# Optimization experiments

Hardware: AMD Instinct MI355X
Metric: run time of the kernel (lower is better)

## Reference

```python
import jax, jax.numpy as jnp
import numpy as np

STEP_SIZE = 0.1
FLOW_STRENGTH = 5.0
MAX_STEPS = 16  # points in [0,1)^2 -> max dist sqrt(2) -> at most floor(14.14)+1 = 15 steps
NNODES = 1024


def setup_inputs() -> dict:
    key = jax.random.key(0)
    ks = jax.random.split(key, 7)
    def lin(k, fan_in, shape):
        bound = 1.0 / np.sqrt(fan_in)
        return jax.random.uniform(k, shape, jnp.float32, -bound, bound)
    return {
        "embedded_points": jax.random.uniform(ks[0], (NNODES, 2), jnp.float32),
        "W1": lin(ks[1], 2, (2, 10)),  "b1": lin(ks[2], 2, (10,)),
        "W2": lin(ks[3], 10, (10, 10)), "b2": lin(ks[4], 10, (10,)),
        "W3": lin(ks[5], 10, (10, 2)),  "b3": lin(ks[6], 10, (2,)),
    }


def _flowfield(x, W1, b1, W2, b2, W3, b3):
    h = jnp.tanh(x @ W1 + b1)
    h = jnp.tanh(h @ W2 + b2)
    return h @ W3 + b3


def reference(embedded_points, W1, b1, W2, b2, W3, b3):
    # Pairwise path-integral cost matrix embedding_D[i, j] = cost(x_i, x_j)
    x1 = embedded_points[:, None, :]            # [n,1,2]
    x2 = embedded_points[None, :, :]            # [1,n,2]
    delta = x2 - x1                              # [n,n,2]
    euc = jnp.linalg.norm(delta, axis=-1)        # [n,n]
    safe_euc = jnp.where(euc > 0, euc, 1.0)
    unit = delta / safe_euc[..., None]           # [n,n,2]

    t = jnp.arange(MAX_STEPS, dtype=embedded_points.dtype)   # [S]
    # steps_to_x2: x1 + t * step_size * (x2-x1)/||x2-x1||   -> [n,n,S,2]
    steps = x1[:, :, None, :] + (t[:, None] * STEP_SIZE) * unit[:, :, None, :]

    flow = _flowfield(steps, W1, b1, W2, b2, W3, b3)          # [n,n,S,2]
    dot = jnp.einsum("ijsd,ijd->ijs", flow, delta)            # [n,n,S]
    e = jnp.exp(dot)
    cost_normalizer = FLOW_STRENGTH * e / (FLOW_STRENGTH - 1.0 + e)
    per_step = STEP_SIZE / cost_normalizer                    # [n,n,S]

    # original loops t in range(int(euc/step_size)+1): valid iff t <= floor(euc/step_size)
    n_valid = jnp.floor(euc / STEP_SIZE)                      # [n,n]
    valid = t[None, None, :] <= n_valid[..., None]            # [n,n,S]
    cost = jnp.sum(jnp.where(valid, per_step, 0.0), axis=-1)  # [n,n]
    # torch.allclose(x1, x2) -> cost 0 (identical points)
    return jnp.where(euc > 0, cost, 0.0)
```

## Files before the change

### kernel.cpp

```cpp
#include <hip/hip_runtime.h>

typedef float v2 __attribute__((ext_vector_type(2)));

constexpr int NN = 1024;
constexpr int GC = 64;
constexpr float GS = 64.0f;
constexpr int NC = GC * GC;

__device__ __forceinline__ v2 splat2(float a) { v2 r; r.x = a; r.y = a; return r; }

__device__ __forceinline__ float fast_tanh(float x) {
    float e = exp2f(x * 2.88539008177792681472f);
    return 1.0f - 2.0f * __builtin_amdgcn_rcpf(1.0f + e);
}

__device__ __forceinline__ v2 mlp_eval(float x, float y,
    const float* __restrict__ W1, const float* __restrict__ b1,
    const float* __restrict__ W2, const float* __restrict__ b2,
    const float* __restrict__ W3, const float* __restrict__ b3)
{
    float h1[10], h2[10];
#pragma unroll
    for (int k = 0; k < 10; ++k)
        h1[k] = fast_tanh(fmaf(x, W1[k], fmaf(y, W1[10 + k], b1[k])));
#pragma unroll
    for (int k = 0; k < 10; ++k) {
        float acc = b2[k];
#pragma unroll
        for (int l = 0; l < 10; ++l) acc = fmaf(h1[l], W2[10 * l + k], acc);
        h2[k] = fast_tanh(acc);
    }
    float f0 = b3[0], f1 = b3[1];
#pragma unroll
    for (int k = 0; k < 10; ++k) {
        f0 = fmaf(h2[k], W3[2 * k], f0);
        f1 = fmaf(h2[k], W3[2 * k + 1], f1);
    }
    v2 r; r.x = f0; r.y = f1;
    return r;
}

__global__ __launch_bounds__(256) void cells_kernel(
    const float* __restrict__ W1, const float* __restrict__ b1,
    const float* __restrict__ W2, const float* __restrict__ b2,
    const float* __restrict__ W3, const float* __restrict__ b3,
    v2* __restrict__ g)
{
    const int c = blockIdx.x * 256 + threadIdx.x;
    if (c >= NC) return;
    const int ix = c & (GC - 1), iy = c >> 6;
    const float x0 = (float)ix * (1.0f / GS), x1 = (float)(ix + 1) * (1.0f / GS);
    const float y0 = (float)iy * (1.0f / GS), y1 = (float)(iy + 1) * (1.0f / GS);

    const v2 f00 = mlp_eval(x0, y0, W1, b1, W2, b2, W3, b3);
    const v2 f10 = mlp_eval(x1, y0, W1, b1, W2, b2, W3, b3);
    const v2 f01 = mlp_eval(x0, y1, W1, b1, W2, b2, W3, b3);

    g[c]          = f00;
    g[NC + c]     = f10 - f00;
    g[2 * NC + c] = f01 - f00;
}

__global__ __launch_bounds__(1024) void flow_kernel(
    const float* __restrict__ pts,
    const v2* __restrict__ g,
    float* __restrict__ out)
{
    __shared__ v2 tab[3 * NC];

    const int t = threadIdx.x;
    {
        const float4* gs = (const float4*)g;
        float4* ls = (float4*)tab;
#pragma unroll
        for (int k = 0; k < 6; ++k)
            ls[t + 1024 * k] = gs[t + 1024 * k];
    }
    __syncthreads();

    const float x2x = pts[2 * t], x2y = pts[2 * t + 1];

#pragma unroll 1
    for (int q = 0; q < 4; ++q) {
        const int i = (blockIdx.x << 2) + q;
        const float x1x = pts[2 * i], x1y = pts[2 * i + 1];
        const float dx = x2x - x1x, dy = x2y - x1y;

        const float nrm2 = __fadd_rn(__fmul_rn(dx, dx), __fmul_rn(dy, dy));
        const float euc  = __fsqrt_rn(nrm2);
        const float se   = (euc > 0.0f) ? euc : 1.0f;
        const float ux   = __fdiv_rn(dx, se), uy = __fdiv_rn(dy, se);
        const int   nvi  = (int)floorf(__fdiv_rn(euc, 0.1f));
        const int   smax = (nvi < 15) ? nvi : 15;

        float pu = x1x * GS, pv = x1y * GS;
        const float du = 6.4f * ux, dv = 6.4f * uy;
        const float dxe = -1.44269504088896340736f * dx;
        const float dye = -1.44269504088896340736f * dy;

        float cost = 0.0f;
#pragma unroll 1
        for (int s = 0; s <= smax; ++s) {
            int ix = (int)pu; ix = (ix < GC - 1) ? ix : (GC - 1);
            int iy = (int)pv; iy = (iy < GC - 1) ? iy : (GC - 1);
            const float tx = pu - (float)ix;
            const float ty = pv - (float)iy;

            const int c = (iy << 6) + ix;
            const v2 a   = tab[c];
            const v2 gdx = tab[NC + c];
            const v2 gdy = tab[2 * NC + c];
            const v2 f = a + splat2(tx) * gdx + splat2(ty) * gdy;

            const float de = fmaf(f.x, dxe, f.y * dye);
            cost += fmaf(0.08f, exp2f(de), 0.02f);

            pu += du; pv += dv;
        }

        out[(i << 10) | t] = (euc > 0.0f) ? cost : 0.0f;
    }
}

extern "C" void kernel_launch(void* const* d_in, const int* in_sizes, int n_in,
                              void* d_out, int out_size, void* d_ws, size_t ws_size,
                              hipStream_t stream) {
    const float* pts = (const float*)d_in[0];
    const float* W1  = (const float*)d_in[1];
    const float* b1  = (const float*)d_in[2];
    const float* W2  = (const float*)d_in[3];
    const float* b2  = (const float*)d_in[4];
    const float* W3  = (const float*)d_in[5];
    const float* b3  = (const float*)d_in[6];
    float* out = (float*)d_out;

    v2* g = (v2*)d_ws;

    cells_kernel<<<NC / 256, 256, 0, stream>>>(W1, b1, W2, b2, W3, b3, g);
    flow_kernel<<<NN / 4, 1024, 0, stream>>>(pts, g, out);
}
```

Baseline: 23.47 us.

## Sort per-block pairs by step count to reduce warp divergence

```diff
diff --git a/kernel.cpp b/kernel.cpp
--- a/kernel.cpp
+++ b/kernel.cpp
@@ -67,23 +67,58 @@
     float* __restrict__ out)
 {
     __shared__ v2 tab[3 * NC];
+    __shared__ v2 ptsL[NN];
+    __shared__ unsigned short ordQ[4 * NN];
+    __shared__ int hist[16];
+    __shared__ int base[16];
 
     const int t = threadIdx.x;
+
     {
         const float4* gs = (const float4*)g;
         float4* ls = (float4*)tab;
 #pragma unroll
         for (int k = 0; k < 6; ++k)
             ls[t + 1024 * k] = gs[t + 1024 * k];
+        ptsL[t] = ((const v2*)pts)[t];
+    }
+    if (t < 16) hist[t] = 0;
+    __syncthreads();
+
+    int myKey[4];
+#pragma unroll
+    for (int q = 0; q < 4; ++q) {
+        const int i = (blockIdx.x << 2) + q;
+        const float ddx = ptsL[t].x - ptsL[i].x;
+        const float ddy = ptsL[t].y - ptsL[i].y;
+        const float n2 = __fadd_rn(__fmul_rn(ddx, ddx), __fmul_rn(ddy, ddy));
+        const float e  = __fsqrt_rn(n2);
+        const int  nv  = (int)floorf(__fdiv_rn(e, 0.1f));
+        myKey[q] = (nv < 15) ? nv : 15;
+        atomicAdd(&hist[myKey[q]], 1);
+    }
+    __syncthreads();
+    if (t == 0) {
+        int acc = 0;
+#pragma unroll
+        for (int k = 0; k < 16; ++k) { base[k] = acc; acc += hist[k]; }
+    }
+    __syncthreads();
+#pragma unroll
+    for (int q = 0; q < 4; ++q) {
+        const int rank = atomicAdd(&base[myKey[q]], 1);
+        ordQ[rank] = (unsigned short)((q << 10) | t);
     }
     __syncthreads();
 
-    const float x2x = pts[2 * t], x2y = pts[2 * t + 1];
+#pragma unroll 1
+    for (int r = 0; r < 4; ++r) {
+        const int item = ordQ[(r << 10) + t];
+        const int q = item >> 10, jj = item & (NN - 1);
+        const int i = (blockIdx.x << 2) + q;
 
-#pragma unroll 1
-    for (int q = 0; q < 4; ++q) {
-        const int i = (blockIdx.x << 2) + q;
-        const float x1x = pts[2 * i], x1y = pts[2 * i + 1];
+        const float x1x = ptsL[i].x,  x1y = ptsL[i].y;
+        const float x2x = ptsL[jj].x, x2y = ptsL[jj].y;
         const float dx = x2x - x1x, dy = x2y - x1y;
 
         const float nrm2 = __fadd_rn(__fmul_rn(dx, dx), __fmul_rn(dy, dy));
@@ -118,7 +153,7 @@
             pu += du; pv += dv;
         }
 
-        out[(i << 10) | t] = (euc > 0.0f) ? cost : 0.0f;
+        out[(i << 10) | jj] = (euc > 0.0f) ? cost : 0.0f;
     }
 }
 
```

Measured after the change: 22.57 us. 1.04x faster.
